# Kernel optimization log

Hardware: AMD Instinct MI355X
Metric: run time of the kernel (lower is better)

## Reference

```python
import jax, jax.numpy as jnp
import numpy as np

N_NODES = 4096
N_EDGES = 16384
D_IN = 128
HID = 1024


def _linear_params(key, fan_in, fan_out):
    kw, kb = jax.random.split(key)
    bound = 1.0 / np.sqrt(fan_in)
    W = jax.random.uniform(kw, (fan_in, fan_out), jnp.float32, -bound, bound)
    b = jax.random.uniform(kb, (fan_out,), jnp.float32, -bound, bound)
    return W, b


def setup_inputs() -> dict:
    key = jax.random.key(0)
    ks = jax.random.split(key, 10)
    H = jax.random.normal(ks[0], (N_NODES, D_IN), jnp.float32)
    e = jax.random.uniform(ks[1], (N_NODES,), jnp.float32)
    # true incidence matrices: one-hot source/destination node per edge
    src = jax.random.randint(ks[2], (N_EDGES,), 0, N_NODES)
    dst = jax.random.randint(ks[3], (N_EDGES,), 0, N_NODES)
    Ro = jax.nn.one_hot(src, N_NODES, dtype=jnp.float32)  # [E, N]
    Ri = jax.nn.one_hot(dst, N_NODES, dtype=jnp.float32)  # [E, N]
    W1, b1 = _linear_params(ks[4], 3 * D_IN, HID)
    W2, b2 = _linear_params(ks[5], HID, HID)
    W3, b3 = _linear_params(ks[6], HID, HID // 2)
    W4, b4 = _linear_params(ks[7], HID // 2, HID // 4)
    W5, b5 = _linear_params(ks[8], HID // 4, 1)
    return {"H": H, "Ro": Ro, "Ri": Ri, "e": e,
            "W1": W1, "b1": b1, "W2": W2, "b2": b2, "W3": W3, "b3": b3,
            "W4": W4, "b4": b4, "W5": W5, "b5": b5}


def reference(H, Ro, Ri, e, W1, b1, W2, b2, W3, b3, W4, b4, W5, b5):
    eH = e[:, None] * H                      # [N, D]
    Ho = Ri.T @ (Ro @ eH)                    # aggregate over edges -> [N, D]
    Hi = Ro.T @ (Ri @ eH)                    # [N, D]
    x = jnp.concatenate([Ho, H, Hi], axis=1)  # [N, 3D]
    x = jnp.tanh(x @ W1 + b1)
    x = jnp.tanh(x @ W2 + b2)
    x = jnp.tanh(x @ W3 + b3)
    x = jnp.tanh(x @ W4 + b4)
    return jax.nn.sigmoid(x @ W5 + b5)       # [N, 1]
```

## Files before the change

kernel.cpp:

```cpp
#include <hip/hip_runtime.h>
#include <hip/hip_bf16.h>
#include <math.h>

#define N_NODES 4096
#define N_EDGES 16384
#define D_IN 128
#define HID 1024

typedef short s8v __attribute__((ext_vector_type(8)));
typedef float f4v __attribute__((ext_vector_type(4)));

__device__ __forceinline__ unsigned short f2b(float v) {
    union { float f; unsigned int u; } c; c.f = v;
    unsigned int u = c.u + 0x7fffu + ((c.u >> 16) & 1u);
    return (unsigned short)(u >> 16);
}
__device__ __forceinline__ void glds16(const unsigned short* g, unsigned short* l) {
    __builtin_amdgcn_global_load_lds(
        (const __attribute__((address_space(1))) void*)g,
        (__attribute__((address_space(3))) void*)l, 16, 0, 0);
}
template<int N> __device__ __forceinline__ void vmcnt_wait() {
    if constexpr (N == 0)      asm volatile("s_waitcnt vmcnt(0)" ::: "memory");
    else if constexpr (N == 4) asm volatile("s_waitcnt vmcnt(4)" ::: "memory");
    else if constexpr (N == 6) asm volatile("s_waitcnt vmcnt(6)" ::: "memory");
    else if constexpr (N == 9) asm volatile("s_waitcnt vmcnt(9)" ::: "memory");
}

__global__ void zero_counts(int* __restrict__ c) {
    c[blockIdx.x * 256 + threadIdx.x] = 0;
}

__global__ void extract_wt(const float* __restrict__ Ro, const float* __restrict__ Ri,
                           int* __restrict__ src_arr, int* __restrict__ dst_arr,
                           int* __restrict__ counts,
                           const float* __restrict__ W1, unsigned short* __restrict__ wt1,
                           const float* __restrict__ W2, unsigned short* __restrict__ wt2,
                           const float* __restrict__ W3, unsigned short* __restrict__ wt3,
                           const float* __restrict__ W4, unsigned short* __restrict__ wt4) {
    int b = blockIdx.x, t = threadIdx.x;
    if (b < 4096) {
        int edge = (b * 256 + t) >> 6;
        int l = t & 63;
        const f4v* ro4 = (const f4v*)(Ro + (size_t)edge * N_NODES);
        const f4v* ri4 = (const f4v*)(Ri + (size_t)edge * N_NODES);
        int src = -1, dst = -1;
        for (int g = 0; g < 4; ++g) {
            f4v va[4], vb[4];
            bool needA = (src < 0), needB = (dst < 0);
            if (needA) {
#pragma unroll
                for (int i = 0; i < 4; ++i)
                    va[i] = __builtin_nontemporal_load(&ro4[(g * 4 + i) * 64 + l]);
            }
            if (needB) {
#pragma unroll
                for (int i = 0; i < 4; ++i)
                    vb[i] = __builtin_nontemporal_load(&ri4[(g * 4 + i) * 64 + l]);
            }
            if (needA) {
#pragma unroll
                for (int i = 0; i < 4; ++i) {
                    if (src < 0) {
                        f4v v = va[i];
                        bool hit = (v.x != 0.0f) | (v.y != 0.0f) | (v.z != 0.0f) | (v.w != 0.0f);
                        unsigned long long m = __ballot(hit);
                        if (m) {
                            int fl = __ffsll((long long)m) - 1;
                            int idx = 0;
                            if (hit) idx = ((g * 4 + i) * 64 + l) * 4 +
                                           (v.x != 0.0f ? 0 : v.y != 0.0f ? 1 : v.z != 0.0f ? 2 : 3);
                            src = __shfl(idx, fl);
                        }
                    }
                }
            }
            if (needB) {
#pragma unroll
                for (int i = 0; i < 4; ++i) {
                    if (dst < 0) {
                        f4v v = vb[i];
                        bool hit = (v.x != 0.0f) | (v.y != 0.0f) | (v.z != 0.0f) | (v.w != 0.0f);
                        unsigned long long m = __ballot(hit);
                        if (m) {
                            int fl = __ffsll((long long)m) - 1;
                            int idx = 0;
                            if (hit) idx = ((g * 4 + i) * 64 + l) * 4 +
                                           (v.x != 0.0f ? 0 : v.y != 0.0f ? 1 : v.z != 0.0f ? 2 : 3);
                            dst = __shfl(idx, fl);
                        }
                    }
                }
            }
            if (src >= 0 && dst >= 0) break;
        }
        if (l == 0) {
            src_arr[edge] = src;
            dst_arr[edge] = dst;
            atomicAdd(&counts[dst], 1);
            atomicAdd(&counts[4096 + src], 1);
        }
        return;
    }
    int wb = b - 4096;
    const float* W; unsigned short* WT; int K, N, tb;
    if (wb < 384)       { W = W1; WT = wt1; K = 384;  N = 1024; tb = wb; }
    else if (wb < 1408) { W = W2; WT = wt2; K = 1024; N = 1024; tb = wb - 384; }
    else if (wb < 1920) { W = W3; WT = wt3; K = 1024; N = 512;  tb = wb - 1408; }
    else                { W = W4; WT = wt4; K = 512;  N = 256;  tb = wb - 1920; }
    __shared__ float tile[32][33];
    int ntx = N >> 5;
    int tk = tb / ntx, tn = tb - tk * ntx;
    int tr = t >> 5, tc = t & 31;
#pragma unroll
    for (int i = 0; i < 4; ++i)
        tile[tr + i * 8][tc] = W[(size_t)(tk * 32 + tr + i * 8) * N + tn * 32 + tc];
    __syncthreads();
#pragma unroll
    for (int i = 0; i < 4; ++i)
        WT[(size_t)(tn * 32 + tr + i * 8) * K + tk * 32 + tc] = f2b(tile[tc][tr + i * 8]);
}

__global__ __launch_bounds__(1024)
void scan_offsets(const int* __restrict__ counts, int* __restrict__ starts,
                  int* __restrict__ cursors) {
    __shared__ int part[1024];
    int t = threadIdx.x;
    for (int a = 0; a < 2; ++a) {
        const int* c = counts + a * 4096;
        int v[4], s = 0;
#pragma unroll
        for (int i = 0; i < 4; ++i) { v[i] = c[t * 4 + i]; s += v[i]; }
        part[t] = s;
        __syncthreads();
        for (int off = 1; off < 1024; off <<= 1) {
            int x = (t >= off) ? part[t - off] : 0;
            __syncthreads();
            part[t] += x;
            __syncthreads();
        }
        int o = part[t] - s;
#pragma unroll
        for (int i = 0; i < 4; ++i) {
            starts[a * 4096 + t * 4 + i]  = o;
            cursors[a * 4096 + t * 4 + i] = o;
            o += v[i];
        }
        __syncthreads();
    }
}

__global__ void fill_lists(const int* __restrict__ src_arr, const int* __restrict__ dst_arr,
                           int* __restrict__ cursors,
                           int* __restrict__ in_list, int* __restrict__ out_list) {
    int e = blockIdx.x * 256 + threadIdx.x;
    int s = src_arr[e], d = dst_arr[e];
    int p = atomicAdd(&cursors[d], 1);
    in_list[p] = e;
    int p2 = atomicAdd(&cursors[4096 + s], 1);
    out_list[p2] = e;
}

__global__ __launch_bounds__(64)
void gather_a1(const float* __restrict__ H, const float* __restrict__ e_arr,
               const int* __restrict__ src_arr, const int* __restrict__ dst_arr,
               const int* __restrict__ starts, const int* __restrict__ counts,
               const int* __restrict__ in_list, const int* __restrict__ out_list,
               unsigned short* __restrict__ A1) {
    int n = blockIdx.x;
    int l = threadIdx.x;
    bool lo = l < 32;
    int f = (lo ? l : l - 32) * 4;
    int base = lo ? starts[n] : starts[4096 + n];
    int cnt  = lo ? counts[n] : counts[4096 + n];
    const int* list  = lo ? in_list : out_list;
    const int* other = lo ? src_arr : dst_arr;
    f4v acc = {0.f, 0.f, 0.f, 0.f};
    for (int i = 0; i < cnt; ++i) {
        int eidx = list[base + i];
        int node = other[eidx];
        float s = e_arr[node];
        f4v h = *(const f4v*)(H + (size_t)node * 128 + f);
        acc.x += s * h.x; acc.y += s * h.y; acc.z += s * h.z; acc.w += s * h.w;
    }
    ushort4 pk;
    pk.x = f2b(acc.x); pk.y = f2b(acc.y); pk.z = f2b(acc.z); pk.w = f2b(acc.w);
    *(ushort4*)&A1[(size_t)n * 384 + (lo ? 0 : 256) + f] = pk;
    if (lo) {
        f4v h = *(const f4v*)(H + (size_t)n * 128 + f);
        ushort4 ph;
        ph.x = f2b(h.x); ph.y = f2b(h.y); ph.z = f2b(h.z); ph.w = f2b(h.w);
        *(ushort4*)&A1[(size_t)n * 384 + 128 + f] = ph;
    }
}

template<int BM, int BN>
__global__ __launch_bounds__(256)
void gemm_db(const unsigned short* __restrict__ A, const unsigned short* __restrict__ BT,
             const float* __restrict__ bias, unsigned short* __restrict__ C,
             int N, int K) {
    constexpr int BK = 64;
    constexpr int MI = BM / 32, NI = BN / 32;
    constexpr int IA = BM / 32, IB = BN / 32, IS = IA + IB;
    __shared__ unsigned short As[2][BM * BK];
    __shared__ unsigned short Bs[2][BN * BK];
    int t = threadIdx.x;
    int l = t & 63, w = t >> 6;
    int wm = w >> 1, wn = w & 1;
    int q = l >> 4, r16 = l & 15;
    int m0 = blockIdx.y * BM, n0 = blockIdx.x * BN;

    f4v acc[MI][NI] = {};

    auto stage = [&](int buf, int k0) {
#pragma unroll
        for (int i = 0; i < IA; ++i) {
            int c = i * 256 + t;
            int row = c >> 3, g = c & 7, gs = g ^ (row & 7);
            glds16(&A[(size_t)(m0 + row) * K + k0 + gs * 8], &As[buf][c * 8]);
        }
#pragma unroll
        for (int i = 0; i < IB; ++i) {
            int c = i * 256 + t;
            int row = c >> 3, g = c & 7, gs = g ^ (row & 7);
            glds16(&BT[(size_t)(n0 + row) * K + k0 + gs * 8], &Bs[buf][c * 8]);
        }
    };

    stage(0, 0);
    int cur = 0;
    for (int k0 = 0; k0 < K; k0 += BK) {
        if (k0 + BK < K) { stage(cur ^ 1, k0 + BK); vmcnt_wait<IS>(); }
        else             { vmcnt_wait<0>(); }
        __builtin_amdgcn_s_barrier();
        s8v a[MI][2], b[NI][2];
#pragma unroll
        for (int mi = 0; mi < MI; ++mi) {
            int row = wm * (BM / 2) + mi * 16 + r16;
#pragma unroll
            for (int kk = 0; kk < 2; ++kk)
                a[mi][kk] = *(const s8v*)&As[cur][row * 64 + ((((kk << 2) | q)) ^ (row & 7)) * 8];
        }
#pragma unroll
        for (int ni = 0; ni < NI; ++ni) {
            int row = wn * (BN / 2) + ni * 16 + r16;
#pragma unroll
            for (int kk = 0; kk < 2; ++kk)
                b[ni][kk] = *(const s8v*)&Bs[cur][row * 64 + ((((kk << 2) | q)) ^ (row & 7)) * 8];
        }
#pragma unroll
        for (int kk = 0; kk < 2; ++kk)
#pragma unroll
            for (int mi = 0; mi < MI; ++mi)
#pragma unroll
                for (int ni = 0; ni < NI; ++ni)
                    acc[mi][ni] = __builtin_amdgcn_mfma_f32_16x16x32_bf16(a[mi][kk], b[ni][kk], acc[mi][ni], 0, 0, 0);
        __builtin_amdgcn_s_barrier();
        cur ^= 1;
    }
#pragma unroll
    for (int mi = 0; mi < MI; ++mi)
#pragma unroll
        for (int ni = 0; ni < NI; ++ni) {
            int col = n0 + wn * (BN / 2) + ni * 16 + r16;
            float bv = bias[col];
#pragma unroll
            for (int r = 0; r < 4; ++r) {
                int row = m0 + wm * (BM / 2) + mi * 16 + q * 4 + r;
                C[(size_t)row * N + col] = f2b(tanhf(acc[mi][ni][r] + bv));
            }
        }
}

__global__ __launch_bounds__(256)
void gemm45(const unsigned short* __restrict__ A, const unsigned short* __restrict__ BT,
            const float* __restrict__ b4, const float* __restrict__ W5,
            const float* __restrict__ b5, float* __restrict__ out) {
    constexpr int BK = 64, K = 512;
    constexpr int NI = 8;
    __shared__ unsigned short As[2][32 * BK];
    __shared__ unsigned short Bs[2][256 * BK];
    __shared__ float part[32][2];
    int t = threadIdx.x;
    int l = t & 63, w = t >> 6;
    int wm = w >> 1, wn = w & 1;
    int q = l >> 4, r16 = l & 15;
    int m0 = blockIdx.y * 32;

    f4v acc[NI] = {};

    auto stage = [&](int buf, int k0) {
        {
            int c = t;
            int row = c >> 3, g = c & 7, gs = g ^ (row & 7);
            glds16(&A[(size_t)(m0 + row) * K + k0 + gs * 8], &As[buf][c * 8]);
        }
#pragma unroll
        for (int i = 0; i < 8; ++i) {
            int c = i * 256 + t;
            int row = c >> 3, g = c & 7, gs = g ^ (row & 7);
            glds16(&BT[(size_t)row * K + k0 + gs * 8], &Bs[buf][c * 8]);
        }
    };

    stage(0, 0);
    int cur = 0;
    for (int k0 = 0; k0 < K; k0 += BK) {
        if (k0 + BK < K) { stage(cur ^ 1, k0 + BK); vmcnt_wait<9>(); }
        else             { vmcnt_wait<0>(); }
        __builtin_amdgcn_s_barrier();
        s8v a[2], b[NI][2];
        {
            int row = wm * 16 + r16;
#pragma unroll
            for (int kk = 0; kk < 2; ++kk)
                a[kk] = *(const s8v*)&As[cur][row * 64 + ((((kk << 2) | q)) ^ (row & 7)) * 8];
        }
#pragma unroll
        for (int ni = 0; ni < NI; ++ni) {
            int row = wn * 128 + ni * 16 + r16;
#pragma unroll
            for (int kk = 0; kk < 2; ++kk)
                b[ni][kk] = *(const s8v*)&Bs[cur][row * 64 + ((((kk << 2) | q)) ^ (row & 7)) * 8];
        }
#pragma unroll
        for (int kk = 0; kk < 2; ++kk)
#pragma unroll
            for (int ni = 0; ni < NI; ++ni)
                acc[ni] = __builtin_amdgcn_mfma_f32_16x16x32_bf16(a[kk], b[ni][kk], acc[ni], 0, 0, 0);
        __builtin_amdgcn_s_barrier();
        cur ^= 1;
    }

    float partial[4] = {0.f, 0.f, 0.f, 0.f};
#pragma unroll
    for (int ni = 0; ni < NI; ++ni) {
        int col = wn * 128 + ni * 16 + r16;
        float bv = b4[col], wv = W5[col];
#pragma unroll
        for (int r = 0; r < 4; ++r)
            partial[r] += tanhf(acc[ni][r] + bv) * wv;
    }
#pragma unroll
    for (int off = 1; off < 16; off <<= 1)
#pragma unroll
        for (int r = 0; r < 4; ++r)
            partial[r] += __shfl_xor(partial[r], off);
    if (r16 == 0)
#pragma unroll
        for (int r = 0; r < 4; ++r)
            part[wm * 16 + q * 4 + r][wn] = partial[r];
    __syncthreads();
    if (t < 32) {
        float s = part[t][0] + part[t][1] + b5[0];
        out[m0 + t] = 1.0f / (1.0f + expf(-s));
    }
}

extern "C" void kernel_launch(void* const* d_in, const int* in_sizes, int n_in,
                              void* d_out, int out_size, void* d_ws, size_t ws_size,
                              hipStream_t stream) {
    const float* H  = (const float*)d_in[0];
    const float* Ro = (const float*)d_in[1];
    const float* Ri = (const float*)d_in[2];
    const float* e  = (const float*)d_in[3];
    const float* W1 = (const float*)d_in[4];  const float* b1 = (const float*)d_in[5];
    const float* W2 = (const float*)d_in[6];  const float* b2 = (const float*)d_in[7];
    const float* W3 = (const float*)d_in[8];  const float* b3 = (const float*)d_in[9];
    const float* W4 = (const float*)d_in[10]; const float* b4 = (const float*)d_in[11];
    const float* W5 = (const float*)d_in[12]; const float* b5 = (const float*)d_in[13];
    float* out = (float*)d_out;

    char* p = (char*)d_ws;
    auto alloc = [&](size_t bytes) -> void* {
        void* r = (void*)p;
        p += (bytes + 255) & ~(size_t)255;
        return r;
    };
    int* counts   = (int*)alloc(8192 * 4);
    int* starts   = (int*)alloc(8192 * 4);
    int* cursors  = (int*)alloc(8192 * 4);
    int* src_arr  = (int*)alloc(N_EDGES * 4);
    int* dst_arr  = (int*)alloc(N_EDGES * 4);
    int* in_list  = (int*)alloc(N_EDGES * 4);
    int* out_list = (int*)alloc(N_EDGES * 4);
    unsigned short* a1  = (unsigned short*)alloc((size_t)N_NODES * 384 * 2);
    unsigned short* h1  = (unsigned short*)alloc((size_t)N_NODES * HID * 2);
    unsigned short* h2  = (unsigned short*)alloc((size_t)N_NODES * HID * 2);
    unsigned short* h3  = (unsigned short*)alloc((size_t)N_NODES * (HID / 2) * 2);
    unsigned short* wt1 = (unsigned short*)alloc((size_t)HID * 384 * 2);
    unsigned short* wt2 = (unsigned short*)alloc((size_t)HID * HID * 2);
    unsigned short* wt3 = (unsigned short*)alloc((size_t)(HID / 2) * HID * 2);
    unsigned short* wt4 = (unsigned short*)alloc((size_t)(HID / 4) * (HID / 2) * 2);

    zero_counts<<<32, 256, 0, stream>>>(counts);

    extract_wt<<<4096 + 2048, 256, 0, stream>>>(Ro, Ri, src_arr, dst_arr, counts,
                                                W1, wt1, W2, wt2, W3, wt3, W4, wt4);

    scan_offsets<<<1, 1024, 0, stream>>>(counts, starts, cursors);

    fill_lists<<<64, 256, 0, stream>>>(src_arr, dst_arr, cursors, in_list, out_list);

    gather_a1<<<N_NODES, 64, 0, stream>>>(H, e, src_arr, dst_arr, starts, counts,
                                          in_list, out_list, a1);

    gemm_db<128, 64><<<dim3(HID / 64, N_NODES / 128), 256, 0, stream>>>(a1, wt1, b1, h1, HID, 384);
    gemm_db<128, 64><<<dim3(HID / 64, N_NODES / 128), 256, 0, stream>>>(h1, wt2, b2, h2, HID, HID);
    gemm_db<64, 64><<<dim3((HID / 2) / 64, N_NODES / 64), 256, 0, stream>>>(h2, wt3, b3, h3, HID / 2, HID);

    gemm45<<<dim3(1, N_NODES / 32), 256, 0, stream>>>(h3, wt4, b4, W5, b5, out);
}
```

Before: 548.0 us.

## Replace CSR scan/fill with fixed-capacity per-node adjacency buckets

Edge extraction now appends each neighbor directly into per-node buckets of fixed capacity via atomic counters, eliminating the prefix-scan and list-fill kernels. The gather reads neighbor node ids directly instead of going through edge indices. This removes two launches, including a single-block serial scan, and one level of indirection. It assumes no node exceeds MAXDEG neighbors, with no overflow check.

```diff
diff --git a/kernel.cpp b/kernel.cpp
--- a/kernel.cpp
+++ b/kernel.cpp
@@ -6,6 +6,7 @@
 #define N_EDGES 16384
 #define D_IN 128
 #define HID 1024
+#define MAXDEG 64
 
 typedef short s8v __attribute__((ext_vector_type(8)));
 typedef float f4v __attribute__((ext_vector_type(4)));
@@ -32,8 +33,9 @@
 }
 
 __global__ void extract_wt(const float* __restrict__ Ro, const float* __restrict__ Ri,
-                           int* __restrict__ src_arr, int* __restrict__ dst_arr,
                            int* __restrict__ counts,
+                           int* __restrict__ in_bucket,
+                           int* __restrict__ out_bucket,
                            const float* __restrict__ W1, unsigned short* __restrict__ wt1,
                            const float* __restrict__ W2, unsigned short* __restrict__ wt2,
                            const float* __restrict__ W3, unsigned short* __restrict__ wt3,
@@ -95,10 +97,10 @@
             if (src >= 0 && dst >= 0) break;
         }
         if (l == 0) {
-            src_arr[edge] = src;
-            dst_arr[edge] = dst;
-            atomicAdd(&counts[dst], 1);
-            atomicAdd(&counts[4096 + src], 1);
+            int s1 = atomicAdd(&counts[dst], 1);
+            in_bucket[dst * MAXDEG + s1] = src;
+            int s2 = atomicAdd(&counts[4096 + src], 1);
+            out_bucket[src * MAXDEG + s2] = dst;
         }
         return;
     }
@@ -121,64 +123,20 @@
         WT[(size_t)(tn * 32 + tr + i * 8) * K + tk * 32 + tc] = f2b(tile[tc][tr + i * 8]);
 }
 
-__global__ __launch_bounds__(1024)
-void scan_offsets(const int* __restrict__ counts, int* __restrict__ starts,
-                  int* __restrict__ cursors) {
-    __shared__ int part[1024];
-    int t = threadIdx.x;
-    for (int a = 0; a < 2; ++a) {
-        const int* c = counts + a * 4096;
-        int v[4], s = 0;
-#pragma unroll
-        for (int i = 0; i < 4; ++i) { v[i] = c[t * 4 + i]; s += v[i]; }
-        part[t] = s;
-        __syncthreads();
-        for (int off = 1; off < 1024; off <<= 1) {
-            int x = (t >= off) ? part[t - off] : 0;
-            __syncthreads();
-            part[t] += x;
-            __syncthreads();
-        }
-        int o = part[t] - s;
-#pragma unroll
-        for (int i = 0; i < 4; ++i) {
-            starts[a * 4096 + t * 4 + i]  = o;
-            cursors[a * 4096 + t * 4 + i] = o;
-            o += v[i];
-        }
-        __syncthreads();
-    }
-}
-
-__global__ void fill_lists(const int* __restrict__ src_arr, const int* __restrict__ dst_arr,
-                           int* __restrict__ cursors,
-                           int* __restrict__ in_list, int* __restrict__ out_list) {
-    int e = blockIdx.x * 256 + threadIdx.x;
-    int s = src_arr[e], d = dst_arr[e];
-    int p = atomicAdd(&cursors[d], 1);
-    in_list[p] = e;
-    int p2 = atomicAdd(&cursors[4096 + s], 1);
-    out_list[p2] = e;
-}
-
 __global__ __launch_bounds__(64)
 void gather_a1(const float* __restrict__ H, const float* __restrict__ e_arr,
-               const int* __restrict__ src_arr, const int* __restrict__ dst_arr,
-               const int* __restrict__ starts, const int* __restrict__ counts,
-               const int* __restrict__ in_list, const int* __restrict__ out_list,
+               const int* __restrict__ counts,
+               const int* __restrict__ in_bucket, const int* __restrict__ out_bucket,
                unsigned short* __restrict__ A1) {
     int n = blockIdx.x;
     int l = threadIdx.x;
     bool lo = l < 32;
     int f = (lo ? l : l - 32) * 4;
-    int base = lo ? starts[n] : starts[4096 + n];
-    int cnt  = lo ? counts[n] : counts[4096 + n];
-    const int* list  = lo ? in_list : out_list;
-    const int* other = lo ? src_arr : dst_arr;
+    int cnt = lo ? counts[n] : counts[4096 + n];
+    const int* bucket = (lo ? in_bucket : out_bucket) + (size_t)n * MAXDEG;
     f4v acc = {0.f, 0.f, 0.f, 0.f};
     for (int i = 0; i < cnt; ++i) {
-        int eidx = list[base + i];
-        int node = other[eidx];
+        int node = bucket[i];
         float s = e_arr[node];
         f4v h = *(const f4v*)(H + (size_t)node * 128 + f);
         acc.x += s * h.x; acc.y += s * h.y; acc.z += s * h.z; acc.w += s * h.w;
@@ -239,14 +197,14 @@
             int row = wm * (BM / 2) + mi * 16 + r16;
 #pragma unroll
             for (int kk = 0; kk < 2; ++kk)
-                a[mi][kk] = *(const s8v*)&As[cur][row * 64 + ((((kk << 2) | q)) ^ (row & 7)) * 8];
+                a[mi][kk] = *(const s8v*)&As[cur][row * 64 + (((kk << 2) | q) ^ (row & 7)) * 8];
         }
 #pragma unroll
         for (int ni = 0; ni < NI; ++ni) {
             int row = wn * (BN / 2) + ni * 16 + r16;
 #pragma unroll
             for (int kk = 0; kk < 2; ++kk)
-                b[ni][kk] = *(const s8v*)&Bs[cur][row * 64 + ((((kk << 2) | q)) ^ (row & 7)) * 8];
+                b[ni][kk] = *(const s8v*)&Bs[cur][row * 64 + (((kk << 2) | q) ^ (row & 7)) * 8];
         }
 #pragma unroll
         for (int kk = 0; kk < 2; ++kk)
@@ -314,14 +272,14 @@
             int row = wm * 16 + r16;
 #pragma unroll
             for (int kk = 0; kk < 2; ++kk)
-                a[kk] = *(const s8v*)&As[cur][row * 64 + ((((kk << 2) | q)) ^ (row & 7)) * 8];
+                a[kk] = *(const s8v*)&As[cur][row * 64 + (((kk << 2) | q) ^ (row & 7)) * 8];
         }
 #pragma unroll
         for (int ni = 0; ni < NI; ++ni) {
             int row = wn * 128 + ni * 16 + r16;
 #pragma unroll
             for (int kk = 0; kk < 2; ++kk)
-                b[ni][kk] = *(const s8v*)&Bs[cur][row * 64 + ((((kk << 2) | q)) ^ (row & 7)) * 8];
+                b[ni][kk] = *(const s8v*)&Bs[cur][row * 64 + (((kk << 2) | q) ^ (row & 7)) * 8];
         }
 #pragma unroll
         for (int kk = 0; kk < 2; ++kk)
@@ -377,13 +335,9 @@
         p += (bytes + 255) & ~(size_t)255;
         return r;
     };
-    int* counts   = (int*)alloc(8192 * 4);
-    int* starts   = (int*)alloc(8192 * 4);
-    int* cursors  = (int*)alloc(8192 * 4);
-    int* src_arr  = (int*)alloc(N_EDGES * 4);
-    int* dst_arr  = (int*)alloc(N_EDGES * 4);
-    int* in_list  = (int*)alloc(N_EDGES * 4);
-    int* out_list = (int*)alloc(N_EDGES * 4);
+    int* counts     = (int*)alloc(8192 * 4);
+    int* in_bucket  = (int*)alloc((size_t)N_NODES * MAXDEG * 4);
+    int* out_bucket = (int*)alloc((size_t)N_NODES * MAXDEG * 4);
     unsigned short* a1  = (unsigned short*)alloc((size_t)N_NODES * 384 * 2);
     unsigned short* h1  = (unsigned short*)alloc((size_t)N_NODES * HID * 2);
     unsigned short* h2  = (unsigned short*)alloc((size_t)N_NODES * HID * 2);
@@ -395,15 +349,10 @@
 
     zero_counts<<<32, 256, 0, stream>>>(counts);
 
-    extract_wt<<<4096 + 2048, 256, 0, stream>>>(Ro, Ri, src_arr, dst_arr, counts,
+    extract_wt<<<4096 + 2048, 256, 0, stream>>>(Ro, Ri, counts, in_bucket, out_bucket,
                                                 W1, wt1, W2, wt2, W3, wt3, W4, wt4);
 
-    scan_offsets<<<1, 1024, 0, stream>>>(counts, starts, cursors);
-
-    fill_lists<<<64, 256, 0, stream>>>(src_arr, dst_arr, cursors, in_list, out_list);
-
-    gather_a1<<<N_NODES, 64, 0, stream>>>(H, e, src_arr, dst_arr, starts, counts,
-                                          in_list, out_list, a1);
+    gather_a1<<<N_NODES, 64, 0, stream>>>(H, e, counts, in_bucket, out_bucket, a1);
 
     gemm_db<128, 64><<<dim3(HID / 64, N_NODES / 128), 256, 0, stream>>>(a1, wt1, b1, h1, HID, 384);
     gemm_db<128, 64><<<dim3(HID / 64, N_NODES / 128), 256, 0, stream>>>(h1, wt2, b2, h2, HID, HID);
```

Measured after the change: 538.6 us. About the same (-1.7%).
